# Kernel optimization log

Hardware: AMD Instinct MI355X
Metric: run time of the kernel (lower is better)

Reference implementation:

```python
import jax, jax.numpy as jnp
import numpy as np

MARGIN = 1.0
TEMPERATURE = 1.0
EPS = 1e-12  # matches torch F.normalize eps default scale behavior (eps=1e-12)


def _l2_normalize(x):
    # torch F.normalize: x / max(||x||, eps)
    norm = jnp.sqrt(jnp.sum(x * x, axis=-1, keepdims=True))
    return x / jnp.maximum(norm, EPS)


def setup_inputs() -> dict:
    key = jax.random.key(0)
    k1, k2 = jax.random.split(key)
    N, D = 8192, 1024
    image_embeds = jax.random.normal(k1, (N, D), dtype=jnp.float32)
    text_embeds = jax.random.normal(k2, (N, D), dtype=jnp.float32)
    return {"image_embeds": image_embeds, "text_embeds": text_embeds}


def reference(image_embeds, text_embeds):
    # L2 normalize; cosine similarity of unit vectors == dot product (GEMM)
    img = _l2_normalize(image_embeds)   # [N, D]
    txt = _l2_normalize(text_embeds)    # [N, D]
    sim = jnp.einsum('nd,md->nm', img, txt) / TEMPERATURE  # [N, N]
    positives = jnp.diagonal(sim)                          # [N]
    # logsumexp over rows of (sim - margin); margin shifts all entries uniformly
    lse = jax.nn.logsumexp(sim - MARGIN, axis=-1)          # [N]
    return jnp.mean(lse - positives)
```

## Files before the change

### kernel.cpp

```cpp
#include <hip/hip_runtime.h>
#include <hip/hip_bf16.h>
#include <stdint.h>

#define N_ROWS 8192
#define DIM    1024
#define BM 128
#define BN 128
#define BKF 128
#define NT (DIM / BKF)
#define TILES_PB 8
#define VSTEPS (NT * TILES_PB)

typedef float   f32x4  __attribute__((ext_vector_type(4)));
typedef int     i32x4  __attribute__((ext_vector_type(4)));
typedef int     i32x8  __attribute__((ext_vector_type(8)));

__device__ __forceinline__ float row_sum16(float x) {
    x += __int_as_float(__builtin_amdgcn_update_dpp(
            0, __float_as_int(x), 0x128 , 0xf, 0xf, true));
    x += __int_as_float(__builtin_amdgcn_update_dpp(
            0, __float_as_int(x), 0x124 , 0xf, 0xf, true));
    x += __int_as_float(__builtin_amdgcn_update_dpp(
            0, __float_as_int(x), 0x122 , 0xf, 0xf, true));
    x += __int_as_float(__builtin_amdgcn_update_dpp(
            0, __float_as_int(x), 0x121 , 0xf, 0xf, true));
    return x;
}

__global__ __launch_bounds__(256) void nrm_kernel(
    const float* __restrict__ img, const float* __restrict__ txt,
    uint8_t* __restrict__ img_f8, uint8_t* __restrict__ txt_f8,
    float* __restrict__ diag, float* __restrict__ S)
{
    const int t    = threadIdx.x;
    const int lane = t & 63;
    const int wv   = t >> 6;
    const int row  = blockIdx.x * 4 + wv;

    const float4* ip = (const float4*)(img + (size_t)row * DIM);
    const float4* tp = (const float4*)(txt + (size_t)row * DIM);

    float4 a[4], b[4];
    float sa = 0.f, sb = 0.f, dp = 0.f;
#pragma unroll
    for (int j = 0; j < 4; ++j) {
        a[j] = ip[lane + 64 * j];
        b[j] = tp[lane + 64 * j];
        sa += a[j].x * a[j].x + a[j].y * a[j].y + a[j].z * a[j].z + a[j].w * a[j].w;
        sb += b[j].x * b[j].x + b[j].y * b[j].y + b[j].z * b[j].z + b[j].w * b[j].w;
        dp += a[j].x * b[j].x + a[j].y * b[j].y + a[j].z * b[j].z + a[j].w * b[j].w;
    }
#pragma unroll
    for (int d = 1; d < 64; d <<= 1) {
        sa += __shfl_xor(sa, d, 64);
        sb += __shfl_xor(sb, d, 64);
        dp += __shfl_xor(dp, d, 64);
    }

    const float ia = 1.0f / fmaxf(sqrtf(sa), 1e-12f);
    const float ib = 1.0f / fmaxf(sqrtf(sb), 1e-12f);

#pragma unroll
    for (int j = 0; j < 4; ++j) {
        int ra = 0, rb = 0;
        ra = __builtin_amdgcn_cvt_pk_fp8_f32(a[j].x * ia, a[j].y * ia, ra, false);
        ra = __builtin_amdgcn_cvt_pk_fp8_f32(a[j].z * ia, a[j].w * ia, ra, true);
        rb = __builtin_amdgcn_cvt_pk_fp8_f32(b[j].x * ib, b[j].y * ib, rb, false);
        rb = __builtin_amdgcn_cvt_pk_fp8_f32(b[j].z * ib, b[j].w * ib, rb, true);
        ((int*)(img_f8 + (size_t)row * DIM))[lane + 64 * j] = ra;
        ((int*)(txt_f8 + (size_t)row * DIM))[lane + 64 * j] = rb;
    }

    if (lane == 0) {
        diag[row] = dp * ia * ib;
        S[row] = 0.0f;
    }
}

__global__ __launch_bounds__(512) void sim_lse_kernel(
    const uint8_t* __restrict__ A, const uint8_t* __restrict__ B,
    float* __restrict__ S)
{
    __shared__ __align__(16) uint8_t smem[2 * 2 * BM * BKF];

    const int t     = threadIdx.x;
    const int lane  = t & 63;
    const int w     = t >> 6;
    const int waveM = w >> 1;
    const int waveN = w & 1;
    const int lr    = lane & 15;
    const int q     = lane >> 4;
    const int swz   = lr & 7;

    const int rowA0 = blockIdx.y * BM;
    const uint8_t* Ablk = A + (size_t)rowA0 * DIM;
    const uint8_t* Bgrp = B + (size_t)blockIdx.x * TILES_PB * BN * DIM;

    const uint32_t lo_off = (uint32_t)(((2 * q) ^ swz) * 16);

    const uint8_t* pA[2];
    const uint8_t* pB[2];
    uint32_t ldsA[2], ldsB[2];
#pragma unroll
    for (int is = 0; is < 2; ++is) {
        const int c   = is * 512 + t;
        const int row = c >> 3;
        const int col = (c & 7) ^ (row & 7);
        pA[is] = Ablk + (size_t)row * DIM + col * 16;
        pB[is] = Bgrp + (size_t)row * DIM + col * 16;
        ldsA[is] = (uint32_t)c * 16;
        ldsB[is] = 16384u + (uint32_t)c * 16;
    }

    auto stage_inc = [&](uint32_t ldsbase) {
#pragma unroll
        for (int is = 0; is < 2; ++is) {
            __builtin_amdgcn_global_load_lds(
                (const __attribute__((address_space(1))) void*)pA[is],
                (__attribute__((address_space(3))) void*)&smem[ldsbase + ldsA[is]],
                16, 0, 0);
            __builtin_amdgcn_global_load_lds(
                (const __attribute__((address_space(1))) void*)pB[is],
                (__attribute__((address_space(3))) void*)&smem[ldsbase + ldsB[is]],
                16, 0, 0);
        }
    };

    const uint32_t adrA  = (uint32_t)((waveM * 32 + lr) * BKF) + lo_off;
    const uint32_t adrAh = (uint32_t)((waveM * 32 + lr) * BKF) + (lo_off ^ 16u);
    const uint32_t adrB  = 16384u + (uint32_t)((waveN * 64 + lr) * BKF) + lo_off;
    const uint32_t adrBh = 16384u + (uint32_t)((waveN * 64 + lr) * BKF) + (lo_off ^ 16u);

    f32x4 acc[2][4] = {};

    stage_inc(0u);
#pragma unroll
    for (int is = 0; is < 2; ++is) { pA[is] += 128; pB[is] += 128; }
    asm volatile("s_waitcnt vmcnt(0)" ::: "memory");
    __builtin_amdgcn_s_barrier();

    const float L2E = 1.44269504088896f;
    const int rowbase = rowA0 + waveM * 32;

    auto compute = [&](uint32_t RBUF) {
        i32x8 af[2], bfr[4];
#pragma unroll
        for (int mi = 0; mi < 2; ++mi) {
            i32x4 lo = *(const i32x4*)&smem[adrA  + RBUF + mi * 2048];
            i32x4 hi = *(const i32x4*)&smem[adrAh + RBUF + mi * 2048];
            af[mi] = __builtin_shufflevector(lo, hi, 0, 1, 2, 3, 4, 5, 6, 7);
        }
#pragma unroll
        for (int ni = 0; ni < 4; ++ni) {
            i32x4 lo = *(const i32x4*)&smem[adrB  + RBUF + ni * 2048];
            i32x4 hi = *(const i32x4*)&smem[adrBh + RBUF + ni * 2048];
            bfr[ni] = __builtin_shufflevector(lo, hi, 0, 1, 2, 3, 4, 5, 6, 7);
        }
#pragma unroll
        for (int mi = 0; mi < 2; ++mi)
#pragma unroll
            for (int ni = 0; ni < 4; ++ni)
                acc[mi][ni] = __builtin_amdgcn_mfma_scale_f32_16x16x128_f8f6f4(
                    af[mi], bfr[ni], acc[mi][ni],
                    0 , 0 ,
                    0, 127 , 0, 127 );
    };

#pragma unroll 1
    for (int p = 0; p < VSTEPS / 2; ++p) {
        stage_inc(32768u);
        {
            const bool wrap = (p & 3) == 3;
            const int dA = wrap ? -(BKF * (NT - 1)) : BKF;
            const int dB = wrap ? (BN * DIM - BKF * (NT - 1)) : BKF;
#pragma unroll
            for (int is = 0; is < 2; ++is) { pA[is] += dA; pB[is] += dB; }
        }
        compute(0u);
        asm volatile("s_waitcnt vmcnt(0)" ::: "memory");
        __builtin_amdgcn_s_barrier();

        if (p < VSTEPS / 2 - 1) {
            stage_inc(0u);
#pragma unroll
            for (int is = 0; is < 2; ++is) { pA[is] += 128; pB[is] += 128; }
        }
        compute(32768u);

        if ((p & 3) == 3) {
#pragma unroll
            for (int mi = 0; mi < 2; ++mi) {
                float p0 = 0.f, p1 = 0.f, p2 = 0.f, p3 = 0.f;
#pragma unroll
                for (int ni = 0; ni < 4; ++ni) {
                    p0 += exp2f(acc[mi][ni].x * L2E - L2E);
                    p1 += exp2f(acc[mi][ni].y * L2E - L2E);
                    p2 += exp2f(acc[mi][ni].z * L2E - L2E);
                    p3 += exp2f(acc[mi][ni].w * L2E - L2E);
                    acc[mi][ni] = (f32x4){0.f, 0.f, 0.f, 0.f};
                }
                p0 = row_sum16(p0); p1 = row_sum16(p1);
                p2 = row_sum16(p2); p3 = row_sum16(p3);
                if ((lane & 15) == 0) {
                    float* dst = &S[rowbase + mi * 16 + (lane >> 4) * 4];
                    atomicAdd(dst + 0, p0); atomicAdd(dst + 1, p1);
                    atomicAdd(dst + 2, p2); atomicAdd(dst + 3, p3);
                }
            }
        }

        asm volatile("s_waitcnt vmcnt(0)" ::: "memory");
        __builtin_amdgcn_s_barrier();
    }
}

__global__ __launch_bounds__(1024) void fin_kernel(
    const float* __restrict__ S, const float* __restrict__ diag,
    float* __restrict__ out)
{
    const int t = threadIdx.x;
    float s = 0.f;
    for (int i = t; i < N_ROWS; i += 1024) s += logf(S[i]) - diag[i];
#pragma unroll
    for (int d = 1; d < 64; d <<= 1) s += __shfl_xor(s, d, 64);
    __shared__ float red[16];
    if ((t & 63) == 0) red[t >> 6] = s;
    __syncthreads();
    if (t == 0) {
        float tot = 0.f;
#pragma unroll
        for (int i = 0; i < 16; ++i) tot += red[i];
        out[0] = tot * (1.0f / N_ROWS);
    }
}

extern "C" void kernel_launch(void* const* d_in, const int* in_sizes, int n_in,
                              void* d_out, int out_size, void* d_ws, size_t ws_size,
                              hipStream_t stream)
{
    const float* img = (const float*)d_in[0];
    const float* txt = (const float*)d_in[1];
    float* out = (float*)d_out;

    char* ws = (char*)d_ws;
    uint8_t* img_f8 = (uint8_t*)ws;
    uint8_t* txt_f8 = (uint8_t*)(ws + (size_t)N_ROWS * DIM);
    float*   S      = (float*)(ws + (size_t)N_ROWS * DIM * 2);
    float*   diag   = S + N_ROWS;

    nrm_kernel<<<N_ROWS / 4, 256, 0, stream>>>(img, txt, img_f8, txt_f8,
                                               diag, S);
    dim3 grid(N_ROWS / BN / TILES_PB, N_ROWS / BM);
    sim_lse_kernel<<<grid, 512, 0, stream>>>(img_f8, txt_f8, S);
    fin_kernel<<<1, 1024, 0, stream>>>(S, diag, out);
}
```

Measured before the change: 179.3 us.

## Switch sim GEMM to 32x32x64 FP8 MFMA with 256-thread blocks

Replaces the 16x16x128 scaled FP8 MFMA with the 32x32x64 variant. Each of four waves now computes a 64x64 sub-tile with 2x2 accumulators. The K-slice drops to 64, giving a new swizzled LDS layout, 256-thread blocks, and 4 column tiles per block (twice the grid). The aim is higher MFMA throughput per LDS fragment and fewer LDS reads per FLOP. The cost is more per-row shuffles and atomics in the exp/sum epilogue and a more complex addressing scheme.

```diff
diff --git a/kernel.cpp b/kernel.cpp
--- a/kernel.cpp
+++ b/kernel.cpp
@@ -6,14 +6,16 @@
 #define DIM    1024
 #define BM 128
 #define BN 128
-#define BKF 128
-#define NT (DIM / BKF)
-#define TILES_PB 8
-#define VSTEPS (NT * TILES_PB)
-
-typedef float   f32x4  __attribute__((ext_vector_type(4)));
-typedef int     i32x4  __attribute__((ext_vector_type(4)));
-typedef int     i32x8  __attribute__((ext_vector_type(8)));
+#define BKF 64
+#define NSL 16
+#define TILES_PB 4
+#define VSTEPS (NSL * TILES_PB)
+#define BUFSZ 16384u
+
+typedef float   f32x4   __attribute__((ext_vector_type(4)));
+typedef float   f32x16  __attribute__((ext_vector_type(16)));
+typedef int     i32x4   __attribute__((ext_vector_type(4)));
+typedef int     i32x8   __attribute__((ext_vector_type(8)));
 
 __device__ __forceinline__ float row_sum16(float x) {
     x += __int_as_float(__builtin_amdgcn_update_dpp(
@@ -77,39 +79,37 @@
     }
 }
 
-__global__ __launch_bounds__(512) void sim_lse_kernel(
+__global__ __launch_bounds__(256) void sim_lse_kernel(
     const uint8_t* __restrict__ A, const uint8_t* __restrict__ B,
     float* __restrict__ S)
 {
-    __shared__ __align__(16) uint8_t smem[2 * 2 * BM * BKF];
+    __shared__ __align__(16) uint8_t smem[2 * BUFSZ];
 
     const int t     = threadIdx.x;
     const int lane  = t & 63;
     const int w     = t >> 6;
     const int waveM = w >> 1;
     const int waveN = w & 1;
-    const int lr    = lane & 15;
-    const int q     = lane >> 4;
-    const int swz   = lr & 7;
+    const int l31   = lane & 31;
 
     const int rowA0 = blockIdx.y * BM;
     const uint8_t* Ablk = A + (size_t)rowA0 * DIM;
     const uint8_t* Bgrp = B + (size_t)blockIdx.x * TILES_PB * BN * DIM;
 
-    const uint32_t lo_off = (uint32_t)(((2 * q) ^ swz) * 16);
-
     const uint8_t* pA[2];
     const uint8_t* pB[2];
     uint32_t ldsA[2], ldsB[2];
 #pragma unroll
     for (int is = 0; is < 2; ++is) {
-        const int c   = is * 512 + t;
-        const int row = c >> 3;
-        const int col = (c & 7) ^ (row & 7);
-        pA[is] = Ablk + (size_t)row * DIM + col * 16;
-        pB[is] = Bgrp + (size_t)row * DIM + col * 16;
-        ldsA[is] = (uint32_t)c * 16;
-        ldsB[is] = 16384u + (uint32_t)c * 16;
+        const int cc   = is * 256 + t;
+        const int vrow = cc >> 3;
+        const int vc   = (cc & 7) ^ (vrow & 7);
+        const int row  = vrow * 2 + (vc >> 2);
+        const int c    = vc & 3;
+        pA[is] = Ablk + (size_t)row * DIM + c * 16;
+        pB[is] = Bgrp + (size_t)row * DIM + c * 16;
+        ldsA[is] = (uint32_t)cc * 16;
+        ldsB[is] = 8192u + (uint32_t)cc * 16;
     }
 
     auto stage_inc = [&](uint32_t ldsbase) {
@@ -126,24 +126,33 @@
         }
     };
 
-    const uint32_t adrA  = (uint32_t)((waveM * 32 + lr) * BKF) + lo_off;
-    const uint32_t adrAh = (uint32_t)((waveM * 32 + lr) * BKF) + (lo_off ^ 16u);
-    const uint32_t adrB  = 16384u + (uint32_t)((waveN * 64 + lr) * BKF) + lo_off;
-    const uint32_t adrBh = 16384u + (uint32_t)((waveN * 64 + lr) * BKF) + (lo_off ^ 16u);
-
-    f32x4 acc[2][4] = {};
+    const uint32_t rkey = (uint32_t)((lane >> 1) & 7);
+    const uint32_t vch0 = (uint32_t)((lane & 1) * 4 + 2 * (lane >> 5));
+    const uint32_t swzc = (vch0 ^ rkey) * 16;
+    const uint32_t adrA  = (uint32_t)((waveM * 32 + (l31 >> 1)) * 128) + swzc;
+    const uint32_t adrAh = adrA ^ 16u;
+    const uint32_t adrB  = 8192u + (uint32_t)((waveN * 32 + (l31 >> 1)) * 128) + swzc;
+    const uint32_t adrBh = adrB ^ 16u;
+
+    f32x16 acc[2][2];
+#pragma unroll
+    for (int mi = 0; mi < 2; ++mi)
+#pragma unroll
+        for (int ni = 0; ni < 2; ++ni)
+#pragma unroll
+            for (int r = 0; r < 16; ++r) acc[mi][ni][r] = 0.f;
 
     stage_inc(0u);
 #pragma unroll
-    for (int is = 0; is < 2; ++is) { pA[is] += 128; pB[is] += 128; }
+    for (int is = 0; is < 2; ++is) { pA[is] += BKF; pB[is] += BKF; }
     asm volatile("s_waitcnt vmcnt(0)" ::: "memory");
     __builtin_amdgcn_s_barrier();
 
     const float L2E = 1.44269504088896f;
-    const int rowbase = rowA0 + waveM * 32;
+    const int rowbase = rowA0 + waveM * 64;
 
     auto compute = [&](uint32_t RBUF) {
-        i32x8 af[2], bfr[4];
+        i32x8 af[2], bf[2];
 #pragma unroll
         for (int mi = 0; mi < 2; ++mi) {
             i32x4 lo = *(const i32x4*)&smem[adrA  + RBUF + mi * 2048];
@@ -151,28 +160,28 @@
             af[mi] = __builtin_shufflevector(lo, hi, 0, 1, 2, 3, 4, 5, 6, 7);
         }
 #pragma unroll
-        for (int ni = 0; ni < 4; ++ni) {
+        for (int ni = 0; ni < 2; ++ni) {
             i32x4 lo = *(const i32x4*)&smem[adrB  + RBUF + ni * 2048];
             i32x4 hi = *(const i32x4*)&smem[adrBh + RBUF + ni * 2048];
-            bfr[ni] = __builtin_shufflevector(lo, hi, 0, 1, 2, 3, 4, 5, 6, 7);
+            bf[ni] = __builtin_shufflevector(lo, hi, 0, 1, 2, 3, 4, 5, 6, 7);
         }
 #pragma unroll
         for (int mi = 0; mi < 2; ++mi)
 #pragma unroll
-            for (int ni = 0; ni < 4; ++ni)
-                acc[mi][ni] = __builtin_amdgcn_mfma_scale_f32_16x16x128_f8f6f4(
-                    af[mi], bfr[ni], acc[mi][ni],
+            for (int ni = 0; ni < 2; ++ni)
+                acc[mi][ni] = __builtin_amdgcn_mfma_scale_f32_32x32x64_f8f6f4(
+                    af[mi], bf[ni], acc[mi][ni],
                     0 , 0 ,
                     0, 127 , 0, 127 );
     };
 
 #pragma unroll 1
     for (int p = 0; p < VSTEPS / 2; ++p) {
-        stage_inc(32768u);
+        stage_inc(BUFSZ);
         {
-            const bool wrap = (p & 3) == 3;
-            const int dA = wrap ? -(BKF * (NT - 1)) : BKF;
-            const int dB = wrap ? (BN * DIM - BKF * (NT - 1)) : BKF;
+            const bool wrap = (p & 7) == 7;
+            const int dA = wrap ? -(BKF * (NSL - 1)) : BKF;
+            const int dB = wrap ? (BN * DIM - BKF * (NSL - 1)) : BKF;
 #pragma unroll
             for (int is = 0; is < 2; ++is) { pA[is] += dA; pB[is] += dB; }
         }
@@ -183,29 +192,28 @@
         if (p < VSTEPS / 2 - 1) {
             stage_inc(0u);
 #pragma unroll
-            for (int is = 0; is < 2; ++is) { pA[is] += 128; pB[is] += 128; }
-        }
-        compute(32768u);
-
-        if ((p & 3) == 3) {
+            for (int is = 0; is < 2; ++is) { pA[is] += BKF; pB[is] += BKF; }
+        }
+        compute(BUFSZ);
+
+        if ((p & 7) == 7) {
 #pragma unroll
             for (int mi = 0; mi < 2; ++mi) {
-                float p0 = 0.f, p1 = 0.f, p2 = 0.f, p3 = 0.f;
-#pragma unroll
-                for (int ni = 0; ni < 4; ++ni) {
-                    p0 += exp2f(acc[mi][ni].x * L2E - L2E);
-                    p1 += exp2f(acc[mi][ni].y * L2E - L2E);
-                    p2 += exp2f(acc[mi][ni].z * L2E - L2E);
-                    p3 += exp2f(acc[mi][ni].w * L2E - L2E);
-                    acc[mi][ni] = (f32x4){0.f, 0.f, 0.f, 0.f};
+#pragma unroll
+                for (int r = 0; r < 16; ++r) {
+                    float e = exp2f(acc[mi][0][r] * L2E - L2E)
+                            + exp2f(acc[mi][1][r] * L2E - L2E);
+                    e = row_sum16(e);
+                    e += __shfl_xor(e, 16, 64);
+                    if (l31 == 0) {
+                        atomicAdd(&S[rowbase + mi * 32 + (r & 3) + 8 * (r >> 2)
+                                     + 4 * (lane >> 5)], e);
+                    }
                 }
-                p0 = row_sum16(p0); p1 = row_sum16(p1);
-                p2 = row_sum16(p2); p3 = row_sum16(p3);
-                if ((lane & 15) == 0) {
-                    float* dst = &S[rowbase + mi * 16 + (lane >> 4) * 4];
-                    atomicAdd(dst + 0, p0); atomicAdd(dst + 1, p1);
-                    atomicAdd(dst + 2, p2); atomicAdd(dst + 3, p3);
-                }
+#pragma unroll
+                for (int ni = 0; ni < 2; ++ni)
+#pragma unroll
+                    for (int r = 0; r < 16; ++r) acc[mi][ni][r] = 0.f;
             }
         }
 
@@ -251,6 +259,6 @@
     nrm_kernel<<<N_ROWS / 4, 256, 0, stream>>>(img, txt, img_f8, txt_f8,
                                                diag, S);
     dim3 grid(N_ROWS / BN / TILES_PB, N_ROWS / BM);
-    sim_lse_kernel<<<grid, 512, 0, stream>>>(img_f8, txt_f8, S);
+    sim_lse_kernel<<<grid, 256, 0, stream>>>(img_f8, txt_f8, S);
     fin_kernel<<<1, 1024, 0, stream>>>(S, diag, out);
 }
```

After: 223.9 us. 24.9% more time.
